# Kernel tuning notes

Measured on AMD Instinct MI355X. Metric: run time of the kernel, lower is better.

## Reference

```python
import jax, jax.numpy as jnp
import numpy as np

B, N, C, O, K, D = 32, 2048, 64, 64, 3, 16

def setup_inputs() -> dict:
    key = jax.random.key(0)
    ks = jax.random.split(key, 6)
    x = jax.random.normal(ks[0], (B, N, C), dtype=jnp.float32)
    node_embeddings = jax.random.normal(ks[1], (N, D), dtype=jnp.float32)
    adj_m = jax.random.uniform(ks[2], (N, N), dtype=jnp.float32)
    weights_pool = jax.random.normal(ks[3], (D, K, C, O), dtype=jnp.float32) * 0.1
    bias_pool = jax.random.normal(ks[4], (D, O), dtype=jnp.float32) * 0.1
    sa_weight = jax.random.normal(ks[5], (N, 2 * N), dtype=jnp.float32) * (1.0 / np.sqrt(2 * N))
    return {"x": x, "node_embeddings": node_embeddings, "adj_m": adj_m,
            "weights_pool": weights_pool, "bias_pool": bias_pool, "sa_weight": sa_weight}

def reference(x, node_embeddings, adj_m, weights_pool, bias_pool, sa_weight):
    n = node_embeddings.shape[0]
    # learned adaptive adjacency [N,N]
    supports = jax.nn.softmax(jax.nn.relu(node_embeddings @ node_embeddings.T), axis=1)
    # SpatialAttention: 1x1 conv over 2N channels == matmul with [N,2N] weight
    z = jnp.concatenate([supports, adj_m], axis=1) @ sa_weight.T  # [N,N]
    s2 = jax.nn.sigmoid(z)
    supports = s2 * adj_m + (1.0 - s2) * supports
    # Chebyshev polynomial basis
    support_set = [jnp.eye(n, dtype=supports.dtype), supports]
    for _ in range(2, K):
        support_set.append(2.0 * supports @ support_set[-1] - support_set[-2])
    supports_k = jnp.stack(support_set, axis=0)  # [K,N,N]
    # per-node generated weights/bias from embeddings
    weights = jnp.einsum('nd,dkio->nkio', node_embeddings, weights_pool)  # [N,K,C,O]
    bias = node_embeddings @ bias_pool  # [N,O]
    # graph conv: aggregate then per-node matmul
    x_g = jnp.einsum('knm,bmc->bnkc', supports_k, x)  # [B,N,K,C]
    x_gconv = jnp.einsum('bnki,nkio->bno', x_g, weights) + bias  # [B,N,O]
    return x_gconv
```

## Files before the change

### kernel.cpp

```cpp
#include <hip/hip_runtime.h>


typedef unsigned short u16;
typedef float f32x4 __attribute__((ext_vector_type(4)));
typedef __bf16 bf16x8 __attribute__((ext_vector_type(8)));
typedef unsigned short u16x8 __attribute__((ext_vector_type(8)));

#define PSTRIDE ((size_t)2048 * 2048)

__device__ __forceinline__ u16 f2bf(float f) {
    unsigned u = __float_as_uint(f);
    u += 0x7FFFu + ((u >> 16) & 1u);
    return (u16)(u >> 16);
}
__device__ __forceinline__ float bf2f(u16 h) {
    return __uint_as_float((unsigned)h << 16);
}
__device__ __forceinline__ void gl_lds16(const void* g, void* l) {
    __builtin_amdgcn_global_load_lds(
        (const __attribute__((address_space(1))) unsigned*)g,
        (__attribute__((address_space(3))) unsigned*)l, 16, 0, 0);
}

__global__ __launch_bounds__(256)
void preamble(const float* __restrict__ E, const float* __restrict__ adj,
              const float* __restrict__ saw, const float* __restrict__ x,
              const float* __restrict__ Wp, const float* __restrict__ bp,
              u16* __restrict__ Acat, u16* __restrict__ sawb,
              u16* __restrict__ xtT, u16* __restrict__ Wpb,
              float* __restrict__ bias) {
    __shared__ float red[4];
    __shared__ u16 t[64][65];
    const int bid = blockIdx.x, tid = threadIdx.x;

    if (bid < 2048) {
        const int n = bid, lane = tid & 63, wave = tid >> 6;
        float e[16];
#pragma unroll
        for (int d = 0; d < 16; ++d) e[d] = E[n * 16 + d];
        float v[8];
        float mx = 0.f;
#pragma unroll
        for (int r = 0; r < 8; ++r) {
            int m = r * 256 + tid;
            const float4* Er = (const float4*)(E + (size_t)m * 16);
            float4 a = Er[0], b = Er[1], c = Er[2], d4 = Er[3];
            float s = 0.f;
            s = fmaf(a.x, e[0], s);  s = fmaf(a.y, e[1], s);
            s = fmaf(a.z, e[2], s);  s = fmaf(a.w, e[3], s);
            s = fmaf(b.x, e[4], s);  s = fmaf(b.y, e[5], s);
            s = fmaf(b.z, e[6], s);  s = fmaf(b.w, e[7], s);
            s = fmaf(c.x, e[8], s);  s = fmaf(c.y, e[9], s);
            s = fmaf(c.z, e[10], s); s = fmaf(c.w, e[11], s);
            s = fmaf(d4.x, e[12], s); s = fmaf(d4.y, e[13], s);
            s = fmaf(d4.z, e[14], s); s = fmaf(d4.w, e[15], s);
            s = fmaxf(s, 0.f);
            v[r] = s;
            mx = fmaxf(mx, s);
        }
        for (int off = 32; off; off >>= 1) mx = fmaxf(mx, __shfl_down(mx, off, 64));
        if (lane == 0) red[wave] = mx;
        __syncthreads();
        mx = fmaxf(fmaxf(red[0], red[1]), fmaxf(red[2], red[3]));
        __syncthreads();
        float sum = 0.f;
#pragma unroll
        for (int r = 0; r < 8; ++r) { v[r] = __expf(v[r] - mx); sum += v[r]; }
        for (int off = 32; off; off >>= 1) sum += __shfl_down(sum, off, 64);
        if (lane == 0) red[wave] = sum;
        __syncthreads();
        sum = red[0] + red[1] + red[2] + red[3];
        float inv = 1.f / sum;
#pragma unroll
        for (int r = 0; r < 8; ++r)
            Acat[(size_t)n * 4096 + r * 256 + tid] = f2bf(v[r] * inv);
    } else if (bid < 6144) {
        size_t j = ((size_t)(bid - 2048) * 256 + tid) * 4;
        float4 v = *(const float4*)(adj + j);
        int n = (int)(j >> 11), c = (int)(j & 2047);
        ushort4 o = make_ushort4(f2bf(v.x), f2bf(v.y), f2bf(v.z), f2bf(v.w));
        *(ushort4*)(Acat + (size_t)n * 4096 + 2048 + c) = o;
    } else if (bid < 14336) {
        size_t j = ((size_t)(bid - 6144) * 256 + tid) * 4;
        float4 v = *(const float4*)(saw + j);
        ushort4 o = make_ushort4(f2bf(v.x), f2bf(v.y), f2bf(v.z), f2bf(v.w));
        *(ushort4*)(sawb + j) = o;
    } else if (bid < 15360) {
        int local = bid - 14336;
        int m0 = (local & 31) * 64, b = local >> 5;
        int c = tid & 63, g = tid >> 6;
#pragma unroll
        for (int r = 0; r < 16; ++r) {
            int mm = g * 16 + r;
            t[mm][c] = f2bf(x[((size_t)b * 2048 + m0 + mm) * 64 + c]);
        }
        __syncthreads();
#pragma unroll
        for (int r = 0; r < 16; ++r) {
            int cc = g * 16 + r;
            xtT[((size_t)b * 64 + cc) * 2048 + m0 + c] = t[c][cc];
        }
    } else {
        int local = bid - 15360;
        if (local < 16) {
            const int d = local;
            const float* base = Wp + (size_t)d * 12288;
            for (int idx = tid; idx < 12288; idx += 256) {
                int o = idx / 192, ki = idx - o * 192;
                int k = ki >> 6, i = ki & 63;
                float v;
                if (k == 0)      v = base[i * 64 + o] - base[2 * 4096 + i * 64 + o];
                else if (k == 1) v = base[4096 + i * 64 + o];
                else             v = 2.f * base[2 * 4096 + i * 64 + o];
                Wpb[(size_t)(d * 64 + o) * 192 + ki] = f2bf(v);
            }
        } else {
            const int nb = local - 16;
#pragma unroll
            for (int it = 0; it < 8; ++it) {
                int idx = tid + it * 256;
                int n = nb * 32 + (idx >> 6), o = idx & 63;
                float s = 0.f;
#pragma unroll
                for (int d = 0; d < 16; ++d) s = fmaf(E[n * 16 + d], bp[d * 64 + o], s);
                bias[(size_t)n * 64 + o] = s;
            }
        }
    }
}

__global__ __launch_bounds__(256, 3)
void gemm_bt(const u16* __restrict__ A, const u16* __restrict__ Bt,
             u16* __restrict__ Cp, int M, int N, int K, int Kh) {
    __shared__ alignas(16) u16 As[128 * 64];
    __shared__ alignas(16) u16 Bs[128 * 64];
    const int tid = threadIdx.x, lane = tid & 63, wave = tid >> 6;
    const int m0 = blockIdx.y * 128, n0 = blockIdx.x * 128;
    const int wm = (wave >> 1) * 64, wn = (wave & 1) * 64;
    const int kbeg = blockIdx.z * Kh, kend = kbeg + Kh;
    const int ml = lane & 15, c0l = lane >> 4;
    f32x4 acc[4][4] = {};

    int baseA[4], mskA[4], baseB[4], mskB[4];
#pragma unroll
    for (int i = 0; i < 4; ++i) { int m = wm + i * 16 + ml; baseA[i] = m * 8; mskA[i] = m & 7; }
#pragma unroll
    for (int j = 0; j < 4; ++j) { int nn = wn + j * 16 + ml; baseB[j] = nn * 8; mskB[j] = nn & 7; }

    for (int k0 = kbeg; k0 < kend; k0 += 64) {
#pragma unroll
        for (int r = 0; r < 4; ++r) {
            int s = wave * 64 + r * 256 + lane;
            int row = s >> 3, gc = (s & 7) ^ (row & 7);
            gl_lds16(A + (size_t)(m0 + row) * K + k0 + gc * 8, As + (size_t)s * 8);
        }
#pragma unroll
        for (int r = 0; r < 4; ++r) {
            int s = wave * 64 + r * 256 + lane;
            int row = s >> 3, gc = (s & 7) ^ (row & 7);
            gl_lds16(Bt + (size_t)(n0 + row) * K + k0 + gc * 8, Bs + (size_t)s * 8);
        }
        __syncthreads();
#pragma unroll
        for (int ks4 = 0; ks4 < 8; ks4 += 4) {
            bf16x8 af[4], bv[4];
#pragma unroll
            for (int i = 0; i < 4; ++i)
                af[i] = *(const bf16x8*)(As + (baseA[i] + ((c0l + ks4) ^ mskA[i])) * 8);
#pragma unroll
            for (int j = 0; j < 4; ++j)
                bv[j] = *(const bf16x8*)(Bs + (baseB[j] + ((c0l + ks4) ^ mskB[j])) * 8);
#pragma unroll
            for (int i = 0; i < 4; ++i)
#pragma unroll
                for (int j = 0; j < 4; ++j)
                    acc[i][j] = __builtin_amdgcn_mfma_f32_16x16x32_bf16(af[i], bv[j], acc[i][j], 0, 0, 0);
        }
        __syncthreads();
    }

    const int col_l = lane & 15, row_l = (lane >> 4) * 4;
    u16* Cz = Cp + (size_t)blockIdx.z * M * N;
#pragma unroll
    for (int i = 0; i < 4; ++i)
#pragma unroll
        for (int j = 0; j < 4; ++j)
#pragma unroll
            for (int r = 0; r < 4; ++r) {
                int row = m0 + wm + i * 16 + row_l + r;
                int col = n0 + wn + j * 16 + col_l;
                Cz[(size_t)row * N + col] = f2bf(acc[i][j][r]);
            }
}

__global__ __launch_bounds__(256)
void reduce_z(const u16* __restrict__ p, const u16* __restrict__ Acat,
              u16* __restrict__ S) {
    size_t j = ((size_t)blockIdx.x * 256 + threadIdx.x) * 4;
    ushort4 p0 = *(const ushort4*)(p + j);
    ushort4 p1 = *(const ushort4*)(p + PSTRIDE + j);
    ushort4 p2 = *(const ushort4*)(p + 2 * PSTRIDE + j);
    ushort4 p3 = *(const ushort4*)(p + 3 * PSTRIDE + j);
    int row = (int)(j >> 11), col = (int)(j & 2047);
    ushort4 sp = *(const ushort4*)(Acat + (size_t)row * 4096 + col);
    ushort4 ad = *(const ushort4*)(Acat + (size_t)row * 4096 + 2048 + col);
    float z0 = bf2f(p0.x) + bf2f(p1.x) + bf2f(p2.x) + bf2f(p3.x);
    float z1 = bf2f(p0.y) + bf2f(p1.y) + bf2f(p2.y) + bf2f(p3.y);
    float z2 = bf2f(p0.z) + bf2f(p1.z) + bf2f(p2.z) + bf2f(p3.z);
    float z3 = bf2f(p0.w) + bf2f(p1.w) + bf2f(p2.w) + bf2f(p3.w);
    float s0 = 1.f / (1.f + __expf(-z0)), s1 = 1.f / (1.f + __expf(-z1));
    float s2 = 1.f / (1.f + __expf(-z2)), s3 = 1.f / (1.f + __expf(-z3));
    ushort4 o = make_ushort4(
        f2bf(s0 * bf2f(ad.x) + (1.f - s0) * bf2f(sp.x)),
        f2bf(s1 * bf2f(ad.y) + (1.f - s1) * bf2f(sp.y)),
        f2bf(s2 * bf2f(ad.z) + (1.f - s2) * bf2f(sp.z)),
        f2bf(s3 * bf2f(ad.w) + (1.f - s3) * bf2f(sp.w)));
    *(ushort4*)(S + j) = o;
}

__global__ __launch_bounds__(256)
void reduceT(const u16* __restrict__ p, u16* __restrict__ xg1b,
             u16* __restrict__ xg1T) {
    __shared__ u16 t[64][68];
    int bx = blockIdx.x * 64, by = blockIdx.y * 64;
    int cg = threadIdx.x & 15, rg = threadIdx.x >> 4;
    int b = bx >> 6;
#pragma unroll
    for (int rr = 0; rr < 4; ++rr) {
        int row = rg * 4 + rr;
        size_t idx = (size_t)(by + row) * 2048 + bx + cg * 4;
        ushort4 q0 = *(const ushort4*)(p + idx);
        ushort4 q1 = *(const ushort4*)(p + PSTRIDE + idx);
        ushort4 q2 = *(const ushort4*)(p + 2 * PSTRIDE + idx);
        ushort4 q3 = *(const ushort4*)(p + 3 * PSTRIDE + idx);
        ushort4 v = make_ushort4(
            f2bf(bf2f(q0.x) + bf2f(q1.x) + bf2f(q2.x) + bf2f(q3.x)),
            f2bf(bf2f(q0.y) + bf2f(q1.y) + bf2f(q2.y) + bf2f(q3.y)),
            f2bf(bf2f(q0.z) + bf2f(q1.z) + bf2f(q2.z) + bf2f(q3.z)),
            f2bf(bf2f(q0.w) + bf2f(q1.w) + bf2f(q2.w) + bf2f(q3.w)));
        *(ushort4*)(xg1b + ((size_t)b * 2048 + by + row) * 64 + cg * 4) = v;
        *(ushort4*)(&t[row][cg * 4]) = v;
    }
    __syncthreads();
    int c = threadIdx.x & 63, g = threadIdx.x >> 6;
#pragma unroll
    for (int r = 0; r < 16; ++r) {
        int row = g * 16 + r;
        xg1T[(size_t)(bx + row) * 2048 + by + c] = t[c][row];
    }
}

__global__ __launch_bounds__(256, 2)
void gconv_mfma(const float* __restrict__ x, const u16* __restrict__ xg1,
                const u16* __restrict__ p, const u16* __restrict__ Wpb,
                const float* __restrict__ bias, const float* __restrict__ E,
                float* __restrict__ out) {
    __shared__ alignas(16) u16 As[128 * 192];
    __shared__ alignas(16) u16 Bs[64 * 192];
    __shared__ float El[16 * 128];
    const int tid = threadIdx.x, lane = tid & 63, wave = tid >> 6;
    const int m0 = blockIdx.x * 128, nb = m0 & 2047, bB = m0 >> 11;
    const int wm = (wave >> 1) * 64, wn = (wave & 1) * 32;
    const int ml = lane & 15, c0l = lane >> 4;
    const int col_l = lane & 15, rl = (lane >> 4) * 4;

#pragma unroll
    for (int it = 0; it < 12; ++it) {
        int s = tid + it * 256;
        int row = s / 24, sc = s - row * 24;
        int gc = (sc & 24) | ((sc ^ row) & 7);
        int grow = m0 + row;
        u16x8 v;
        if (gc < 8) {
            const float* xp = x + (size_t)grow * 64 + gc * 8;
            float4 a = *(const float4*)xp, b4 = *(const float4*)(xp + 4);
            v[0] = f2bf(a.x);  v[1] = f2bf(a.y);  v[2] = f2bf(a.z);  v[3] = f2bf(a.w);
            v[4] = f2bf(b4.x); v[5] = f2bf(b4.y); v[6] = f2bf(b4.z); v[7] = f2bf(b4.w);
        } else if (gc < 16) {
            v = *(const u16x8*)(xg1 + (size_t)grow * 64 + (gc & 7) * 8);
        } else {
            int n = grow & 2047, c8 = (gc & 7) * 8;
            const u16* pp = p + (size_t)n * 2048 + bB * 64 + c8;
            u16x8 q0 = *(const u16x8*)pp;
            u16x8 q1 = *(const u16x8*)(pp + PSTRIDE);
            u16x8 q2 = *(const u16x8*)(pp + 2 * PSTRIDE);
            u16x8 q3 = *(const u16x8*)(pp + 3 * PSTRIDE);
#pragma unroll
            for (int tt = 0; tt < 8; ++tt)
                v[tt] = f2bf(bf2f(q0[tt]) + bf2f(q1[tt]) + bf2f(q2[tt]) + bf2f(q3[tt]));
        }
        *(u16x8*)(As + (size_t)s * 8) = v;
    }
#pragma unroll
    for (int it = 0; it < 8; ++it) {
        int idx = tid + it * 256;
        El[idx] = E[(size_t)(nb + (idx & 127)) * 16 + (idx >> 7)];
    }
    f32x4 oacc[4][2];
#pragma unroll
    for (int i = 0; i < 4; ++i)
#pragma unroll
        for (int j = 0; j < 2; ++j)
#pragma unroll
            for (int r = 0; r < 4; ++r)
                oacc[i][j][r] = bias[(size_t)(nb + wm + i * 16 + rl + r) * 64 + wn + j * 16 + col_l];
    __syncthreads();

    bf16x8 af[4][6];
#pragma unroll
    for (int i = 0; i < 4; ++i) {
        int m = wm + i * 16 + ml, base = m * 24, msk = m & 7;
#pragma unroll
        for (int ks = 0; ks < 6; ++ks) {
            int c = c0l + ks * 4;
            af[i][ks] = *(const bf16x8*)(As + (base + ((c & 24) | ((c ^ msk) & 7))) * 8);
        }
    }

    for (int d = 0; d < 16; ++d) {
        if (d) __syncthreads();
#pragma unroll
        for (int it = 0; it < 6; ++it) {
            int s = tid + it * 256;
            int row = s / 24, sc = s - row * 24;
            int gc = (sc & 24) | ((sc ^ row) & 7);
            gl_lds16(Wpb + (size_t)(d * 64 + row) * 192 + gc * 8, Bs + (size_t)s * 8);
        }
        __syncthreads();
        f32x4 tmp[4][2] = {};
#pragma unroll
        for (int ks = 0; ks < 6; ++ks) {
            bf16x8 bv[2];
#pragma unroll
            for (int j = 0; j < 2; ++j) {
                int o = wn + j * 16 + ml, msk = o & 7, c = c0l + ks * 4;
                bv[j] = *(const bf16x8*)(Bs + (o * 24 + ((c & 24) | ((c ^ msk) & 7))) * 8);
            }
#pragma unroll
            for (int i = 0; i < 4; ++i)
#pragma unroll
                for (int j = 0; j < 2; ++j)
                    tmp[i][j] = __builtin_amdgcn_mfma_f32_16x16x32_bf16(af[i][ks], bv[j], tmp[i][j], 0, 0, 0);
        }
#pragma unroll
        for (int i = 0; i < 4; ++i)
#pragma unroll
            for (int r = 0; r < 4; ++r) {
                float ev = El[d * 128 + wm + i * 16 + rl + r];
#pragma unroll
                for (int j = 0; j < 2; ++j)
                    oacc[i][j][r] = fmaf(ev, tmp[i][j][r], oacc[i][j][r]);
            }
    }
#pragma unroll
    for (int i = 0; i < 4; ++i)
#pragma unroll
        for (int j = 0; j < 2; ++j)
#pragma unroll
            for (int r = 0; r < 4; ++r)
                out[(size_t)(m0 + wm + i * 16 + rl + r) * 64 + wn + j * 16 + col_l] = oacc[i][j][r];
}

extern "C" void kernel_launch(void* const* d_in, const int* in_sizes, int n_in,
                              void* d_out, int out_size, void* d_ws, size_t ws_size,
                              hipStream_t stream) {
    const float* x   = (const float*)d_in[0];
    const float* E   = (const float*)d_in[1];
    const float* adj = (const float*)d_in[2];
    const float* Wp  = (const float*)d_in[3];
    const float* bp  = (const float*)d_in[4];
    const float* saw = (const float*)d_in[5];
    float* out = (float*)d_out;

    char* ws = (char*)d_ws;
    const size_t MB = 1u << 20;
    u16*   Acat  = (u16*)(ws);
    u16*   sawb  = (u16*)(ws + 16 * MB);
    u16*   XtT   = (u16*)(ws + 32 * MB);
    u16*   Wpb   = (u16*)(ws + 40 * MB);
    float* bias  = (float*)(ws + 41 * MB);
    u16*   part  = (u16*)(ws + 48 * MB);
    u16*   S_bf  = (u16*)(ws + 16 * MB);
    u16*   xg1T  = (u16*)(ws + 24 * MB);
    u16*   xg1b  = (u16*)(ws);

    preamble<<<15440, 256, 0, stream>>>(E, adj, saw, x, Wp, bp, Acat, sawb, XtT, Wpb, bias);

    gemm_bt<<<dim3(16, 16, 4), 256, 0, stream>>>(Acat, sawb, part, 2048, 2048, 4096, 1024);
    reduce_z<<<4096, 256, 0, stream>>>(part, Acat, S_bf);
    gemm_bt<<<dim3(16, 16, 4), 256, 0, stream>>>(S_bf, XtT, part, 2048, 2048, 2048, 512);
    reduceT<<<dim3(32, 32), 256, 0, stream>>>(part, xg1b, xg1T);
    gemm_bt<<<dim3(16, 16, 4), 256, 0, stream>>>(S_bf, xg1T, part, 2048, 2048, 2048, 512);

    gconv_mfma<<<512, 256, 0, stream>>>(x, xg1b, part, Wpb, bias, E, out);
}
```

Measured before the change: 288.1 us.

## Double-buffer weight tiles in reused LDS and stage embeddings through shared memory

In the graph-conv kernel the separate Bs weight buffer is dropped. Per-d weight tiles are now double-buffered inside the As region, which is free once the A fragments sit in registers. The next tile's async global-to-LDS load is issued before the current tile's MFMAs, hiding load latency and removing one barrier per iteration. The preamble softmax now loads embedding rows coalesced into padded LDS rather than as per-thread strided float4 reads, at the cost of two extra barriers per row chunk.

```diff
diff --git a/kernel.cpp b/kernel.cpp
--- a/kernel.cpp
+++ b/kernel.cpp
@@ -31,6 +31,7 @@
               float* __restrict__ bias) {
     __shared__ float red[4];
     __shared__ u16 t[64][65];
+    __shared__ float Ep[256 * 17];
     const int bid = blockIdx.x, tid = threadIdx.x;
 
     if (bid < 2048) {
@@ -40,20 +41,21 @@
         for (int d = 0; d < 16; ++d) e[d] = E[n * 16 + d];
         float v[8];
         float mx = 0.f;
-#pragma unroll
         for (int r = 0; r < 8; ++r) {
-            int m = r * 256 + tid;
-            const float4* Er = (const float4*)(E + (size_t)m * 16);
-            float4 a = Er[0], b = Er[1], c = Er[2], d4 = Er[3];
+            __syncthreads();
+#pragma unroll
+            for (int it = 0; it < 4; ++it) {
+                int flat = it * 1024 + tid * 4;
+                float4 val = *(const float4*)(E + r * 4096 + flat);
+                int row = flat >> 4, col = flat & 15;
+                float* dst = Ep + row * 17 + col;
+                dst[0] = val.x; dst[1] = val.y; dst[2] = val.z; dst[3] = val.w;
+            }
+            __syncthreads();
+            const float* er = Ep + tid * 17;
             float s = 0.f;
-            s = fmaf(a.x, e[0], s);  s = fmaf(a.y, e[1], s);
-            s = fmaf(a.z, e[2], s);  s = fmaf(a.w, e[3], s);
-            s = fmaf(b.x, e[4], s);  s = fmaf(b.y, e[5], s);
-            s = fmaf(b.z, e[6], s);  s = fmaf(b.w, e[7], s);
-            s = fmaf(c.x, e[8], s);  s = fmaf(c.y, e[9], s);
-            s = fmaf(c.z, e[10], s); s = fmaf(c.w, e[11], s);
-            s = fmaf(d4.x, e[12], s); s = fmaf(d4.y, e[13], s);
-            s = fmaf(d4.z, e[14], s); s = fmaf(d4.w, e[15], s);
+#pragma unroll
+            for (int c = 0; c < 16; ++c) s = fmaf(er[c], e[c], s);
             s = fmaxf(s, 0.f);
             v[r] = s;
             mx = fmaxf(mx, s);
@@ -256,7 +258,6 @@
                 const float* __restrict__ bias, const float* __restrict__ E,
                 float* __restrict__ out) {
     __shared__ alignas(16) u16 As[128 * 192];
-    __shared__ alignas(16) u16 Bs[64 * 192];
     __shared__ float El[16 * 128];
     const int tid = threadIdx.x, lane = tid & 63, wave = tid >> 6;
     const int m0 = blockIdx.x * 128, nb = m0 & 2047, bB = m0 >> 11;
@@ -316,17 +317,29 @@
             af[i][ks] = *(const bf16x8*)(As + (base + ((c & 24) | ((c ^ msk) & 7))) * 8);
         }
     }
+    __syncthreads();
+
+#pragma unroll
+    for (int it = 0; it < 6; ++it) {
+        int s = tid + it * 256;
+        int row = s / 24, sc = s - row * 24;
+        int gc = (sc & 24) | ((sc ^ row) & 7);
+        gl_lds16(Wpb + (size_t)row * 192 + gc * 8, As + (size_t)s * 8);
+    }
 
     for (int d = 0; d < 16; ++d) {
-        if (d) __syncthreads();
-#pragma unroll
-        for (int it = 0; it < 6; ++it) {
-            int s = tid + it * 256;
-            int row = s / 24, sc = s - row * 24;
-            int gc = (sc & 24) | ((sc ^ row) & 7);
-            gl_lds16(Wpb + (size_t)(d * 64 + row) * 192 + gc * 8, Bs + (size_t)s * 8);
-        }
-        __syncthreads();
+        __syncthreads();
+        if (d < 15) {
+            u16* nbuf = As + ((d + 1) & 1) * (64 * 192);
+#pragma unroll
+            for (int it = 0; it < 6; ++it) {
+                int s = tid + it * 256;
+                int row = s / 24, sc = s - row * 24;
+                int gc = (sc & 24) | ((sc ^ row) & 7);
+                gl_lds16(Wpb + (size_t)((d + 1) * 64 + row) * 192 + gc * 8, nbuf + (size_t)s * 8);
+            }
+        }
+        const u16* Bs = As + (d & 1) * (64 * 192);
         f32x4 tmp[4][2] = {};
 #pragma unroll
         for (int ks = 0; ks < 6; ++ks) {
```

Measured after the change: 291.1 us. About the same (+1.0%).
